# Kernel optimization log

Hardware: AMD Instinct MI355X
Metric: run time of the kernel (lower is better)

The kernel has to match this reference:

```python
import jax, jax.numpy as jnp
import numpy as np

GROUPS = 4      # DySample groups (default)
DSTATE = 16     # SSM state size
BN_EPS = 1e-5


def grid_sample_border(img, grid):
    # img: (N, C, H, W); grid: (N, Ho, Wo, 2), xy order, [-1, 1], align_corners=False,
    # padding_mode='border' (coords clamped before bilinear interp).
    N, C, H, W = img.shape
    x = jnp.clip((grid[..., 0] + 1.0) * (W * 0.5) - 0.5, 0.0, W - 1.0)
    y = jnp.clip((grid[..., 1] + 1.0) * (H * 0.5) - 0.5, 0.0, H - 1.0)
    x0 = jnp.floor(x); y0 = jnp.floor(y)
    wx = (x - x0)[:, None]; wy = (y - y0)[:, None]          # (N,1,Ho,Wo)
    x0i = x0.astype(jnp.int32); y0i = y0.astype(jnp.int32)
    x1i = jnp.minimum(x0i + 1, W - 1); y1i = jnp.minimum(y0i + 1, H - 1)
    gat = jax.vmap(lambda im, yy, xx: im[:, yy, xx])        # (C,H,W),(Ho,Wo)->(C,Ho,Wo)
    v00 = gat(img, y0i, x0i); v01 = gat(img, y0i, x1i)
    v10 = gat(img, y1i, x0i); v11 = gat(img, y1i, x1i)
    return v00 * (1 - wx) * (1 - wy) + v01 * wx * (1 - wy) + v10 * (1 - wx) * wy + v11 * wx * wy


def dysample(x, off_w, off_b, scale):
    # DySample 'lp' style (ICCV'23), groups=4, no dyscope.
    B, C, H, W = x.shape
    s, g = scale, GROUPS
    conv = jnp.einsum('bchw,co->bohw', x, off_w) + off_b[None, :, None, None]  # (B, 2*g*s*s, H, W)
    hh = ((jnp.arange(s) - (s - 1) / 2.0) / s).astype(x.dtype)                 # subpixel init positions
    ip_x = jnp.broadcast_to(hh[None, None, :], (g, s, s))
    ip_y = jnp.broadcast_to(hh[None, :, None], (g, s, s))
    ip = jnp.stack([ip_x, ip_y])                                               # (2, g, s, s)
    off = conv.reshape(B, 2, g, s, s, H, W) * 0.25 + ip[None, :, :, :, :, None, None]
    cx = jnp.arange(W, dtype=x.dtype) + 0.5
    cy = jnp.arange(H, dtype=x.dtype) + 0.5
    gx = 2.0 * (cx + off[:, 0]) / W - 1.0                                      # (B,g,s,s,H,W)
    gy = 2.0 * (cy[:, None] + off[:, 1]) / H - 1.0
    # pixel_shuffle: (B,g,si,sj,H,W) -> (B,g,H,si,W,sj) -> (B,g,sH,sW)
    gx = gx.transpose(0, 1, 4, 2, 5, 3).reshape(B, g, s * H, s * W)
    gy = gy.transpose(0, 1, 4, 2, 5, 3).reshape(B, g, s * H, s * W)
    grid = jnp.stack([gx, gy], -1).reshape(B * g, s * H, s * W, 2)
    xg = x.reshape(B * g, C // g, H, W)
    return grid_sample_border(xg, grid).reshape(B, C, s * H, s * W)


def channel_ssm(x, in_w, in_b, xproj_w, dt_w, dt_b, A_log, Dp, out_w, out_b):
    # Channel-wise bidirectional selective scan (S6) over the channel axis, gating x.
    B, C, H, W = x.shape
    n = DSTATE
    s = x.mean((-2, -1))                            # (B, C) channel descriptor
    u = s[..., None] * in_w + in_b                  # (B, C, d)
    proj = u @ xproj_w                              # (B, C, 1 + 2n)
    dt_raw = proj[..., :1]
    Bs = proj[..., 1:1 + n]
    Cs = proj[..., 1 + n:]
    dt = jax.nn.softplus(dt_raw * dt_w + dt_b)      # (B, C, d)
    A = -jnp.exp(A_log)                             # (d, n)
    dA = jnp.exp(dt[..., None] * A)                 # (B, C, d, n)
    dBu = (dt * u)[..., None] * Bs[:, :, None, :]   # (B, C, d, n)

    def scan_dir(dA_, dBu_, Cs_):
        def step(h, inp):
            a, b, c = inp
            h = a * h + b                           # (B, d, n)
            return h, jnp.einsum('bdn,bn->bd', h, c)
        h0 = jnp.zeros((B, dA_.shape[2], n), x.dtype)
        _, ys = jax.lax.scan(step, h0, (jnp.swapaxes(dA_, 0, 1), jnp.swapaxes(dBu_, 0, 1), jnp.swapaxes(Cs_, 0, 1)))
        return jnp.swapaxes(ys, 0, 1)               # (B, C, d)

    y = scan_dir(dA, dBu, Cs)
    y = y + scan_dir(dA[:, ::-1], dBu[:, ::-1], Cs[:, ::-1])[:, ::-1]
    y = y + Dp * u
    gate = jax.nn.sigmoid(y @ out_w + out_b)        # (B, C)
    return x * gate[:, :, None, None]


def setup_inputs():
    key = jax.random.key(0)
    ks = jax.random.split(key, 24)
    f = jnp.float32
    rn = lambda k, shp, sc=1.0: jax.random.normal(k, shp, dtype=f) * sc
    B = 2
    inp = {}
    inp['c1'] = rn(ks[0], (B, 96, 128, 128))
    inp['c2'] = rn(ks[1], (B, 96, 64, 64))
    inp['c3'] = rn(ks[2], (B, 192, 32, 32))
    inp['c4'] = rn(ks[3], (B, 384, 16, 16))
    inp['mlp1_w'] = rn(ks[4], (96, 384), 0.05); inp['mlp1_b'] = jnp.zeros((384,), f)
    inp['mlp2_w'] = rn(ks[5], (96, 384), 0.05); inp['mlp2_b'] = jnp.zeros((384,), f)
    inp['mlp3_w'] = rn(ks[6], (192, 384), 0.05); inp['mlp3_b'] = jnp.zeros((384,), f)
    inp['mlp4_w'] = rn(ks[7], (384, 384), 0.05); inp['mlp4_b'] = jnp.zeros((384,), f)
    inp['up2_w'] = rn(ks[8], (384, 2 * 4 * 4), 0.001); inp['up2_b'] = jnp.zeros((2 * 4 * 4,), f)
    inp['up4_w'] = rn(ks[9], (384, 2 * 4 * 16), 0.001); inp['up4_b'] = jnp.zeros((2 * 4 * 16,), f)
    inp['up8_w'] = rn(ks[10], (384, 2 * 4 * 64), 0.001); inp['up8_b'] = jnp.zeros((2 * 4 * 64,), f)
    inp['ssm_in_w'] = rn(ks[11], (64,), 0.5); inp['ssm_in_b'] = rn(ks[12], (64,), 0.1)
    inp['ssm_xproj_w'] = rn(ks[13], (64, 1 + 2 * 16), 0.1)
    inp['ssm_dt_w'] = rn(ks[14], (64,), 0.1); inp['ssm_dt_b'] = jnp.full((64,), -2.0, f)
    inp['ssm_A_log'] = jnp.log(jnp.broadcast_to(jnp.arange(1, 17, dtype=f), (64, 16)))
    inp['ssm_D'] = jnp.ones((64,), f)
    inp['ssm_out_w'] = rn(ks[15], (64,), 0.1); inp['ssm_out_b'] = jnp.zeros((), f)
    inp['fuse_w'] = rn(ks[16], (1536, 384), 0.02)
    inp['bn_g'] = jnp.ones((384,), f); inp['bn_b'] = jnp.zeros((384,), f)
    inp['bn_m'] = jnp.zeros((384,), f); inp['bn_v'] = jnp.ones((384,), f)
    inp['pred_w'] = rn(ks[17], (384, 6), 0.05); inp['pred_b'] = jnp.zeros((6,), f)
    inp['bird_w'] = rn(ks[18], (384, 2), 0.05); inp['bird_b'] = jnp.zeros((2,), f)
    return inp


def reference(c1, c2, c3, c4, mlp1_w, mlp1_b, mlp2_w, mlp2_b, mlp3_w, mlp3_b, mlp4_w, mlp4_b,
              up2_w, up2_b, up4_w, up4_b, up8_w, up8_b,
              ssm_in_w, ssm_in_b, ssm_xproj_w, ssm_dt_w, ssm_dt_b, ssm_A_log, ssm_D, ssm_out_w, ssm_out_b,
              fuse_w, bn_g, bn_b, bn_m, bn_v, pred_w, pred_b, bird_w, bird_b):
    proj = lambda c, w, b: jnp.einsum('bchw,ce->behw', c, w) + b[None, :, None, None]
    _c4 = dysample(proj(c4, mlp4_w, mlp4_b), up8_w, up8_b, 8)
    _c3 = dysample(proj(c3, mlp3_w, mlp3_b), up4_w, up4_b, 4)
    _c2 = dysample(proj(c2, mlp2_w, mlp2_b), up2_w, up2_b, 2)
    _c1 = proj(c1, mlp1_w, mlp1_b)
    cc = jnp.concatenate([_c4, _c3, _c2, _c1], axis=1)      # (B, 1536, 128, 128)
    cc = channel_ssm(cc, ssm_in_w, ssm_in_b, ssm_xproj_w, ssm_dt_w, ssm_dt_b, ssm_A_log, ssm_D, ssm_out_w, ssm_out_b)
    h = jnp.einsum('bchw,co->bohw', cc, fuse_w)             # 1x1 conv, no bias
    h = (h - bn_m[None, :, None, None]) * (bn_g / jnp.sqrt(bn_v + BN_EPS))[None, :, None, None] + bn_b[None, :, None, None]
    h = jax.nn.relu(h)                                      # dropout = identity (eval)
    out = jnp.einsum('bchw,co->bohw', h, pred_w) + pred_b[None, :, None, None]
    aux = jnp.einsum('bchw,co->bohw', h, bird_w) + bird_b[None, :, None, None]
    return (out, aux)
```

## Files before the change

### kernel.cpp

```cpp
#include <hip/hip_runtime.h>
#include <cstddef>

#define HWO 16384
#define CTOT 1536

typedef __attribute__((ext_vector_type(8))) short bf16x8;
typedef __attribute__((ext_vector_type(4))) float f32x4;

__device__ inline unsigned short f2bf(float x) {
  union { float f; unsigned u; } v; v.f = x;
  unsigned r = v.u + 0x7FFFu + ((v.u >> 16) & 1u);
  return (unsigned short)(r >> 16);
}
__device__ inline float bf2f(unsigned short h) {
  union { unsigned u; float f; } v; v.u = ((unsigned)h) << 16; return v.f;
}

struct __align__(16) Prm { unsigned short i00, i01, i10, i11; float wx, wy; };

struct SetupArgs {
  const float* W[7];
  unsigned short* T[7];
  int K[7], N[7], bstart[8];
  const float *bn_g, *bn_v, *bn_m, *bn_b;
  float *sc, *sh;
  const float* c1;
  float* mc1;
  const float* fw;
  unsigned short* fwt;
  int nTP;
};
__global__ __launch_bounds__(256) void setup_kernel(SetupArgs a) {
  int bid = blockIdx.x;
  if (bid < a.nTP) {
    int s = 0;
#pragma unroll
    for (int i = 1; i < 7; i++) if (bid >= a.bstart[i]) s = i;
    const int K = a.K[s], N = a.N[s];
    const int idx = (bid - a.bstart[s]) * 256 + threadIdx.x;
    if (idx >= K * N) return;
    const int k = idx / N, o = idx - k * N;
    a.T[s][(size_t)o * K + k] = f2bf(a.W[s][idx]);
    return;
  }
  bid -= a.nTP;
  if (bid < 2) {
    const int o = bid * 256 + threadIdx.x;
    if (o < 384) {
      const float sc = a.bn_g[o] * rsqrtf(a.bn_v[o] + 1e-5f);
      a.sc[o] = sc;
      a.sh[o] = a.bn_b[o] - a.bn_m[o] * sc;
    }
    return;
  }
  bid -= 2;
  if (bid < 192) {
    const float4* p = (const float4*)(a.c1 + (size_t)bid * HWO);
    float acc = 0.f;
    for (int i = threadIdx.x; i < HWO / 4; i += 256) {
      const float4 v = p[i];
      acc += (v.x + v.y) + (v.z + v.w);
    }
    for (int o = 32; o > 0; o >>= 1) acc += __shfl_down(acc, o, 64);
    __shared__ float red[4];
    if ((threadIdx.x & 63) == 0) red[threadIdx.x >> 6] = acc;
    __syncthreads();
    if (threadIdx.x == 0)
      a.mc1[bid] = (red[0] + red[1] + red[2] + red[3]) * (1.0f / HWO);
    return;
  }
  bid -= 192;
  const int tk = bid / 12, to = bid % 12;
  __shared__ float tile[32][33];
  const int rr0 = threadIdx.x >> 5, cch = threadIdx.x & 31;
#pragma unroll
  for (int rr = rr0; rr < 32; rr += 8)
    tile[rr][cch] = a.fw[(size_t)(tk * 32 + rr) * 384 + to * 32 + cch];
  __syncthreads();
#pragma unroll
  for (int rr = rr0; rr < 32; rr += 8)
    a.fwt[(size_t)(to * 32 + rr) * 1536 + tk * 32 + cch] = f2bf(tile[cch][rr]);
}

struct PSeg { const float* X; const unsigned short* Wt; const float* bias;
              unsigned short* Y; int P, K, blk0; };
struct PArgs { PSeg s[4]; };
__global__ __launch_bounds__(256) void proj_all(PArgs a) {
  int si = 0;
#pragma unroll
  for (int i = 1; i < 4; i++) if ((int)blockIdx.x >= a.s[i].blk0) si = i;
  const PSeg sg = a.s[si];
  const int rel = blockIdx.x - sg.blk0;
  const int pb = rel >> 1, ob = rel & 1;
  const int b = blockIdx.y;
  const int P = sg.P, K = sg.K;
  const int p0 = pb * 128;
  constexpr int LST = 40;
  __shared__ unsigned short Alds[128 * LST];
  __shared__ unsigned short Blds[192 * LST];
  const int tid = threadIdx.x;
  const int w = tid >> 6, lane = tid & 63;
  const int wm = w >> 1, wn = w & 1;
  const float* Xf = sg.X + (long)b * K * P;
  const unsigned short* Wt = sg.Wt;
  f32x4 acc[24];
#pragma unroll
  for (int i = 0; i < 24; i++) acc[i] = (f32x4){0.f, 0.f, 0.f, 0.f};
  const int lr = lane & 15, lk = (lane >> 4) * 8;

  for (int kc = 0; kc < K; kc += 32) {
#pragma unroll
    for (int it = 0; it < 4; it++) {
      const int idx = tid + it * 256;
      const int k = idx >> 5, pg = (idx & 31) * 4;
      const float4 v = *(const float4*)(Xf + (long)(kc + k) * P + p0 + pg);
      Alds[(pg + 0) * LST + k] = f2bf(v.x);
      Alds[(pg + 1) * LST + k] = f2bf(v.y);
      Alds[(pg + 2) * LST + k] = f2bf(v.z);
      Alds[(pg + 3) * LST + k] = f2bf(v.w);
    }
#pragma unroll
    for (int it = 0; it < 3; it++) {
      const int idx = tid + it * 256;
      const int r = idx >> 2, ck = (idx & 3) * 8;
      *(uint4*)&Blds[r * LST + ck] =
          *(const uint4*)(Wt + (long)(ob * 192 + r) * K + kc + ck);
    }
    __syncthreads();
    bf16x8 af[4];
#pragma unroll
    for (int mt = 0; mt < 4; mt++)
      af[mt] = *(const bf16x8*)&Alds[((wm * 4 + mt) * 16 + lr) * LST + lk];
#pragma unroll
    for (int ot = 0; ot < 6; ot++) {
      const bf16x8 bfr = *(const bf16x8*)&Blds[((wn * 6 + ot) * 16 + lr) * LST + lk];
#pragma unroll
      for (int mt = 0; mt < 4; mt++)
        acc[mt * 6 + ot] = __builtin_amdgcn_mfma_f32_16x16x32_bf16(
            af[mt], bfr, acc[mt * 6 + ot], 0, 0, 0);
    }
    __syncthreads();
  }
  const int r0 = (lane >> 4) * 4;
#pragma unroll
  for (int mt = 0; mt < 4; mt++) {
#pragma unroll
    for (int ot = 0; ot < 6; ot++) {
      const int o = ob * 192 + (wn * 6 + ot) * 16 + lr;
      const float bv = sg.bias[o];
      const f32x4 r = acc[mt * 6 + ot];
#pragma unroll
      for (int jj = 0; jj < 4; jj++) {
        const long row = p0 + (wm * 4 + mt) * 16 + r0 + jj;
        sg.Y[((long)b * P + row) * 384 + o] = f2bf(r[jj] + bv);
      }
    }
  }
}

struct OSeg { const unsigned short* X; const unsigned short* Wt;
              const float* bias; float* Y; int P, N, obn, blk0; };
struct OArgs { OSeg s[3]; };
__global__ __launch_bounds__(256) void offs_all(OArgs a) {
  int si = 0;
#pragma unroll
  for (int i = 1; i < 3; i++) if ((int)blockIdx.x >= a.s[i].blk0) si = i;
  const OSeg sg = a.s[si];
  const int rel = blockIdx.x - sg.blk0;
  const int pb = rel / sg.obn, ob = rel - pb * sg.obn;
  const int b = blockIdx.y;
  const int P = sg.P, N = sg.N;
  const int p0 = pb * 128, o0 = ob * 128;
  constexpr int LST = 40;
  __shared__ unsigned short Alds[128 * LST];
  __shared__ unsigned short Blds[128 * LST];
  const int tid = threadIdx.x;
  const int w = tid >> 6, lane = tid & 63;
  const int wm = w >> 1, wn = w & 1;
  const unsigned short* Xb = sg.X + (long)b * P * 384;
  f32x4 acc[16];
#pragma unroll
  for (int i = 0; i < 16; i++) acc[i] = (f32x4){0.f, 0.f, 0.f, 0.f};
  const int lr = lane & 15, lk = (lane >> 4) * 8;

  for (int kc = 0; kc < 384; kc += 32) {
#pragma unroll
    for (int it = 0; it < 2; it++) {
      const int idx = tid + it * 256;
      const int r = idx >> 2, ck = (idx & 3) * 8;
      *(uint4*)&Alds[r * LST + ck] =
          *(const uint4*)(Xb + (long)(p0 + r) * 384 + kc + ck);
    }
#pragma unroll
    for (int it = 0; it < 2; it++) {
      const int idx = tid + it * 256;
      const int r = idx >> 2, ck = (idx & 3) * 8;
      uint4 v = {0u, 0u, 0u, 0u};
      if (o0 + r < N)
        v = *(const uint4*)(sg.Wt + (long)(o0 + r) * 384 + kc + ck);
      *(uint4*)&Blds[r * LST + ck] = v;
    }
    __syncthreads();
    bf16x8 af[4];
#pragma unroll
    for (int mt = 0; mt < 4; mt++)
      af[mt] = *(const bf16x8*)&Alds[((wm * 4 + mt) * 16 + lr) * LST + lk];
#pragma unroll
    for (int ot = 0; ot < 4; ot++) {
      const bf16x8 bfr = *(const bf16x8*)&Blds[((wn * 4 + ot) * 16 + lr) * LST + lk];
#pragma unroll
      for (int mt = 0; mt < 4; mt++)
        acc[mt * 4 + ot] = __builtin_amdgcn_mfma_f32_16x16x32_bf16(
            af[mt], bfr, acc[mt * 4 + ot], 0, 0, 0);
    }
    __syncthreads();
  }
  const int r0 = (lane >> 4) * 4;
#pragma unroll
  for (int mt = 0; mt < 4; mt++) {
#pragma unroll
    for (int ot = 0; ot < 4; ot++) {
      const int o = o0 + (wn * 4 + ot) * 16 + lr;
      if (o < N) {
        const float bv = sg.bias[o];
        const f32x4 r = acc[mt * 4 + ot];
#pragma unroll
        for (int jj = 0; jj < 4; jj++) {
          const long row = p0 + (wm * 4 + mt) * 16 + r0 + jj;
          sg.Y[((long)b * P + row) * N + o] = r[jj] + bv;
        }
      }
    }
  }
}

__global__ __launch_bounds__(256) void pm_kernel(
    const float* __restrict__ bo4, const float* __restrict__ bo3,
    const float* __restrict__ bo2,
    const unsigned short* __restrict__ bp4, const unsigned short* __restrict__ bp3,
    const unsigned short* __restrict__ bp2,
    Prm* __restrict__ prm, float* __restrict__ part) {
  const int gp = blockIdx.y, b = blockIdx.z;
  const int lvl = gp >> 2, g = gp & 3;
  const float* bo; int ls, H, offC;
  const unsigned short* bpL; int HWs_;
  if (lvl == 0)      { bo = bo4; ls = 3; H = 16; offC = 512; bpL = bp4; HWs_ = 256; }
  else if (lvl == 1) { bo = bo3; ls = 2; H = 32; offC = 128; bpL = bp3; HWs_ = 1024; }
  else               { bo = bo2; ls = 1; H = 64; offC = 32;  bpL = bp2; HWs_ = 4096; }
  const int s = 1 << ls, ss = s * s, W = H;
  const int tid = threadIdx.x;
  __shared__ Prm Plds[512];

#pragma unroll
  for (int ii = 0; ii < 2; ii++) {
    const int li = tid + ii * 256;
    const int p = blockIdx.x * 512 + li;
    const int yo = p >> 7, xo = p & 127;
    const int h = yo >> ls, i = yo & (s - 1);
    const int w = xo >> ls, j = xo & (s - 1);
    const int sp = h * W + w;
    const float* offp = bo + ((size_t)b * (W * H) + sp) * offC;
    const float cx = offp[g * ss + i * s + j];
    const float cy = offp[(4 + g) * ss + i * s + j];
    const float inv_s = 1.0f / (float)s;
    const float offx = cx * 0.25f + ((float)j - (s - 1) * 0.5f) * inv_s;
    const float offy = cy * 0.25f + ((float)i - (s - 1) * 0.5f) * inv_s;
    float xf = fminf(fmaxf((float)w + offx, 0.0f), (float)(W - 1));
    float yf = fminf(fmaxf((float)h + offy, 0.0f), (float)(H - 1));
    const float x0f = floorf(xf), y0f = floorf(yf);
    const int x0 = (int)x0f, y0 = (int)y0f;
    const int x1 = min(x0 + 1, W - 1), y1 = min(y0 + 1, H - 1);
    Prm pr;
    pr.i00 = (unsigned short)(y0 * W + x0);
    pr.i01 = (unsigned short)(y0 * W + x1);
    pr.i10 = (unsigned short)(y1 * W + x0);
    pr.i11 = (unsigned short)(y1 * W + x1);
    pr.wx = xf - x0f;
    pr.wy = yf - y0f;
    prm[((size_t)b * 12 + gp) * HWO + p] = pr;
    Plds[li] = pr;
  }
  __syncthreads();

  const int chunk = tid % 12, pl = tid / 12;
  float acc[8];
#pragma unroll
  for (int j = 0; j < 8; j++) acc[j] = 0.f;
  const unsigned short* qb = bpL + (size_t)b * HWs_ * 384 + g * 96 + chunk * 8;
  if (tid < 252) {
    for (int it = 0; it < 25; it++) {
      const int pli = it * 21 + pl;
      if (pli < 512) {
        const Prm pr = Plds[pli];
        const float wx = pr.wx, wy = pr.wy;
        const float w00 = (1.f - wx) * (1.f - wy), w01 = wx * (1.f - wy);
        const float w10 = (1.f - wx) * wy, w11 = wx * wy;
        const uint4 v00 = *(const uint4*)(qb + (size_t)pr.i00 * 384);
        const uint4 v01 = *(const uint4*)(qb + (size_t)pr.i01 * 384);
        const uint4 v10 = *(const uint4*)(qb + (size_t)pr.i10 * 384);
        const uint4 v11 = *(const uint4*)(qb + (size_t)pr.i11 * 384);
        const unsigned short* s00 = (const unsigned short*)&v00;
        const unsigned short* s01 = (const unsigned short*)&v01;
        const unsigned short* s10 = (const unsigned short*)&v10;
        const unsigned short* s11 = (const unsigned short*)&v11;
#pragma unroll
        for (int j = 0; j < 8; j++)
          acc[j] += w00 * bf2f(s00[j]) + w01 * bf2f(s01[j]) +
                    w10 * bf2f(s10[j]) + w11 * bf2f(s11[j]);
      }
    }
  }
  __shared__ float red[12][8][22];
  if (tid < 252) {
#pragma unroll
    for (int j = 0; j < 8; j++) red[chunk][j][pl] = acc[j];
  }
  __syncthreads();
  if (tid < 96) {
    float sum = 0.f;
#pragma unroll
    for (int l = 0; l < 21; l++) sum += red[tid >> 3][tid & 7][l];
    part[((size_t)blockIdx.x * 2 + b) * 1152 + gp * 96 + tid] = sum;
  }
}

__global__ __launch_bounds__(64) void ssm_prep(
    const float* __restrict__ part, const float* __restrict__ mc1,
    const float* __restrict__ mlp1_w, const float* __restrict__ mlp1_b,
    const float* __restrict__ in_w, const float* __restrict__ in_b,
    const float* __restrict__ xproj_w, const float* __restrict__ dt_w,
    const float* __restrict__ dt_b, float* __restrict__ u_out,
    float2* __restrict__ dtdu_out, float* __restrict__ Bs_out,
    float* __restrict__ Cs_out) {
  const int bc = blockIdx.x;
  const int b = bc / 1536, c = bc - b * 1536;
  const int d = threadIdx.x;
  float sv;
  if (c < 1152) {
    float a = (d < 32) ? part[((size_t)d * 2 + b) * 1152 + c] : 0.f;
    a += __shfl_xor(a, 1, 64);  a += __shfl_xor(a, 2, 64);
    a += __shfl_xor(a, 4, 64);  a += __shfl_xor(a, 8, 64);
    a += __shfl_xor(a, 16, 64); a += __shfl_xor(a, 32, 64);
    sv = a * (1.0f / HWO);
  } else {
    const int c2 = c - 1152;
    float a = mc1[b * 96 + d] * mlp1_w[d * 384 + c2];
    if (d < 32) a += mc1[b * 96 + 64 + d] * mlp1_w[(64 + d) * 384 + c2];
    a += __shfl_xor(a, 1, 64);  a += __shfl_xor(a, 2, 64);
    a += __shfl_xor(a, 4, 64);  a += __shfl_xor(a, 8, 64);
    a += __shfl_xor(a, 16, 64); a += __shfl_xor(a, 32, 64);
    sv = a + mlp1_b[c2];
  }
  const float u = sv * in_w[d] + in_b[d];
  __shared__ float ush[64];
  __shared__ float proj[33];
  ush[d] = u;
  __syncthreads();
  if (d < 33) {
    float acc = 0.f;
    for (int k = 0; k < 64; k++) acc = fmaf(ush[k], xproj_w[k * 33 + d], acc);
    proj[d] = acc;
  }
  __syncthreads();
  float dtv = proj[0] * dt_w[d] + dt_b[d];
  dtv = (dtv > 20.0f) ? dtv : log1pf(__expf(dtv));
  u_out[(size_t)bc * 64 + d] = u;
  dtdu_out[(size_t)bc * 64 + d] = make_float2(dtv, dtv * u);
  if (d < 16) {
    Bs_out[(size_t)bc * 16 + d] = proj[1 + d];
    Cs_out[(size_t)bc * 16 + d] = proj[17 + d];
  }
}

__global__ __launch_bounds__(256) void ssm_scan_par(
    const float2* __restrict__ dtdu, const float* __restrict__ Bs,
    const float* __restrict__ Cs, const float* __restrict__ A_log,
    float* __restrict__ y) {
  const int d = blockIdx.x, dir = blockIdx.y, b = blockIdx.z;
  const int t = threadIdx.x;
  const int j = t >> 4, n = t & 15;
  const float A = -__expf(A_log[d * 16 + n]);
  const int s0 = j * 96;
  const int c0 = dir ? (1535 - s0) : s0;
  const int step = dir ? -1 : 1;
  const float2* dbase = dtdu + (size_t)b * 1536 * 64 + (size_t)c0 * 64 + d;
  const float* bbase = Bs + (size_t)b * 1536 * 16 + (size_t)c0 * 16 + n;
  const float* cbase = Cs + (size_t)b * 1536 * 16 + (size_t)c0 * 16 + n;
  const long dstep = (long)step * 64;
  const long bstep = (long)step * 16;

  float Ap = 1.f, Bp = 0.f;
  {
    const float2* dp = dbase;
    const float* bp = bbase;
    float2 td = *dp;
    float Bv = *bp;
    for (int i = 0; i < 96; i++) {
      const float2 tdc = td;
      const float Bc = Bv;
      dp += dstep; bp += bstep;
      if (i + 1 < 96) { td = *dp; Bv = *bp; }
      const float a = __expf(tdc.x * A);
      Bp = fmaf(a, Bp, tdc.y * Bc);
      Ap *= a;
    }
  }
  __shared__ float sA[16][16], sB[16][16];
  sA[j][n] = Ap;
  sB[j][n] = Bp;
  __syncthreads();
  float H = 0.f;
  for (int jj = 0; jj < j; jj++) H = fmaf(sA[jj][n], H, sB[jj][n]);

  float* yb = y + (size_t)(b * 2 + dir) * 1536 * 64;
  {
    const float2* dp = dbase;
    const float* bp = bbase;
    const float* cp = cbase;
    float2 td = *dp;
    float Bv = *bp;
    float Cv = *cp;
    float h = H;
    int c = c0;
    for (int i = 0; i < 96; i++) {
      const float2 tdc = td;
      const float Bc = Bv, Cc = Cv;
      dp += dstep; bp += bstep; cp += bstep;
      if (i + 1 < 96) { td = *dp; Bv = *bp; Cv = *cp; }
      const float a = __expf(tdc.x * A);
      h = fmaf(a, h, tdc.y * Bc);
      float pr = h * Cc;
      pr += __shfl_xor(pr, 1, 64);
      pr += __shfl_xor(pr, 2, 64);
      pr += __shfl_xor(pr, 4, 64);
      pr += __shfl_xor(pr, 8, 64);
      if (n == 0) yb[(size_t)c * 64 + d] = pr;
      c += step;
    }
  }
}

__global__ __launch_bounds__(64) void gate_kernel(
    const float* __restrict__ y, const float* __restrict__ u,
    const float* __restrict__ Dp, const float* __restrict__ out_w,
    const float* __restrict__ out_b, float* __restrict__ gate) {
  const int c = blockIdx.x, b = blockIdx.y, d = threadIdx.x;
  const size_t i = ((size_t)b * 1536 + c) * 64 + d;
  float yt = y[((size_t)(b * 2) * 1536 + c) * 64 + d]
           + y[((size_t)(b * 2 + 1) * 1536 + c) * 64 + d]
           + Dp[d] * u[i];
  float v = yt * out_w[d];
  for (int o = 32; o > 0; o >>= 1) v += __shfl_down(v, o, 64);
  if (d == 0) gate[b * 1536 + c] = 1.0f / (1.0f + __expf(-(v + out_b[0])));
}

__global__ __launch_bounds__(256) void gate_fold(
    const unsigned short* __restrict__ wtf, const float* __restrict__ gate,
    unsigned short* __restrict__ wg) {
  const int b = blockIdx.y;
  const int idx8 = blockIdx.x * 256 + threadIdx.x;
  const int o = idx8 / 192;
  const int k0 = (idx8 - o * 192) * 8;
  const size_t idx = (size_t)o * 1536 + k0;
  const uint4 v = *(const uint4*)(wtf + idx);
  const unsigned short* s = (const unsigned short*)&v;
  const float* g = gate + b * 1536 + k0;
  unsigned short r8[8];
#pragma unroll
  for (int j = 0; j < 8; j++) r8[j] = f2bf(bf2f(s[j]) * g[j]);
  *(uint4*)(wg + (size_t)b * 589824 + idx) = *(const uint4*)r8;
}

__global__ __launch_bounds__(1024, 4) void fuse_gemm(
    const unsigned short* __restrict__ bp4, const unsigned short* __restrict__ bp3,
    const unsigned short* __restrict__ bp2, const unsigned short* __restrict__ bp1,
    const Prm* __restrict__ prm, const unsigned short* __restrict__ wg,
    const float* __restrict__ ep_a, const float* __restrict__ ep_b,
    unsigned short* __restrict__ hbf) {
  constexpr int LST = 36;
  __shared__ unsigned short Alds[128 * LST];
  __shared__ unsigned short Blds[384 * LST];
  const int tid = threadIdx.x;
  const int w = tid >> 6, lane = tid & 63;
  const int wm = w >> 2, wn = w & 3;
  const int b = blockIdx.y;
  const int p0 = blockIdx.x * 128;
  const unsigned short* Wb = wg + (size_t)b * 589824;
  f32x4 acc[12];
#pragma unroll
  for (int i = 0; i < 12; i++) acc[i] = (f32x4){0.f, 0.f, 0.f, 0.f};
  const int lr = lane & 15, lk = (lane >> 4) * 8;
  const int ar = tid >> 2, ag = tid & 3;

  for (int gp = 0; gp < 12; ++gp) {
    const int lvl = gp >> 2;
    const unsigned short* bpL; int HWs_;
    if (lvl == 0)      { bpL = bp4; HWs_ = 256; }
    else if (lvl == 1) { bpL = bp3; HWs_ = 1024; }
    else               { bpL = bp2; HWs_ = 4096; }
    Prm pr; pr.i00 = pr.i01 = pr.i10 = pr.i11 = 0; pr.wx = pr.wy = 0.f;
    if (tid < 512) pr = prm[((size_t)b * 12 + gp) * HWO + p0 + ar];
    const float wx = pr.wx, wy = pr.wy;
    const float w00 = (1.f - wx) * (1.f - wy), w01 = wx * (1.f - wy);
    const float w10 = (1.f - wx) * wy, w11 = wx * wy;
#pragma unroll
    for (int t3 = 0; t3 < 3; ++t3) {
      const int kc = gp * 96 + t3 * 32;
      if (tid < 512) {
        const int colL = (gp & 3) * 96 + t3 * 32 + ag * 8;
        const unsigned short* qb = bpL + (size_t)b * HWs_ * 384 + colL;
        const uint4 v00 = *(const uint4*)(qb + (size_t)pr.i00 * 384);
        const uint4 v01 = *(const uint4*)(qb + (size_t)pr.i01 * 384);
        const uint4 v10 = *(const uint4*)(qb + (size_t)pr.i10 * 384);
        const uint4 v11 = *(const uint4*)(qb + (size_t)pr.i11 * 384);
        const unsigned short* s00 = (const unsigned short*)&v00;
        const unsigned short* s01 = (const unsigned short*)&v01;
        const unsigned short* s10 = (const unsigned short*)&v10;
        const unsigned short* s11 = (const unsigned short*)&v11;
        unsigned short r8[8];
#pragma unroll
        for (int jj = 0; jj < 8; jj++)
          r8[jj] = f2bf(w00 * bf2f(s00[jj]) + w01 * bf2f(s01[jj]) +
                        w10 * bf2f(s10[jj]) + w11 * bf2f(s11[jj]));
        *(uint4*)&Alds[ar * LST + ag * 8] = *(const uint4*)r8;
      }
      {
        const int r = tid >> 2, ck = (tid & 3) * 8;
        *(uint4*)&Blds[r * LST + ck] =
            *(const uint4*)(Wb + (size_t)r * 1536 + kc + ck);
      }
      if (tid >= 512) {
        const int idx = tid + 512;
        const int r = idx >> 2, ck = (idx & 3) * 8;
        *(uint4*)&Blds[r * LST + ck] =
            *(const uint4*)(Wb + (size_t)r * 1536 + kc + ck);
      }
      __syncthreads();
      bf16x8 af[2];
#pragma unroll
      for (int mt = 0; mt < 2; mt++)
        af[mt] = *(const bf16x8*)&Alds[((wm * 2 + mt) * 16 + lr) * LST + lk];
#pragma unroll
      for (int ot = 0; ot < 6; ot++) {
        const bf16x8 bfr = *(const bf16x8*)&Blds[((wn * 6 + ot) * 16 + lr) * LST + lk];
#pragma unroll
        for (int mt = 0; mt < 2; mt++)
          acc[mt * 6 + ot] = __builtin_amdgcn_mfma_f32_16x16x32_bf16(
              af[mt], bfr, acc[mt * 6 + ot], 0, 0, 0);
      }
      __syncthreads();
    }
  }
  for (int kc = 1152; kc < 1536; kc += 32) {
    if (tid < 512)
      *(uint4*)&Alds[ar * LST + ag * 8] =
          *(const uint4*)(bp1 + ((size_t)b * HWO + p0 + ar) * 384 +
                          (kc - 1152) + ag * 8);
    {
      const int r = tid >> 2, ck = (tid & 3) * 8;
      *(uint4*)&Blds[r * LST + ck] =
          *(const uint4*)(Wb + (size_t)r * 1536 + kc + ck);
    }
    if (tid >= 512) {
      const int idx = tid + 512;
      const int r = idx >> 2, ck = (idx & 3) * 8;
      *(uint4*)&Blds[r * LST + ck] =
          *(const uint4*)(Wb + (size_t)r * 1536 + kc + ck);
    }
    __syncthreads();
    bf16x8 af[2];
#pragma unroll
    for (int mt = 0; mt < 2; mt++)
      af[mt] = *(const bf16x8*)&Alds[((wm * 2 + mt) * 16 + lr) * LST + lk];
#pragma unroll
    for (int ot = 0; ot < 6; ot++) {
      const bf16x8 bfr = *(const bf16x8*)&Blds[((wn * 6 + ot) * 16 + lr) * LST + lk];
#pragma unroll
      for (int mt = 0; mt < 2; mt++)
        acc[mt * 6 + ot] = __builtin_amdgcn_mfma_f32_16x16x32_bf16(
            af[mt], bfr, acc[mt * 6 + ot], 0, 0, 0);
    }
    __syncthreads();
  }
  const int r0 = (lane >> 4) * 4;
#pragma unroll
  for (int mt = 0; mt < 2; mt++) {
#pragma unroll
    for (int ot = 0; ot < 6; ot++) {
      const int o = (wn * 6 + ot) * 16 + lr;
      const float sa = ep_a[o], sb = ep_b[o];
      const f32x4 r = acc[mt * 6 + ot];
#pragma unroll
      for (int jj = 0; jj < 4; jj++) {
        const size_t row = p0 + (wm * 2 + mt) * 16 + r0 + jj;
        hbf[((size_t)b * HWO + row) * 384 + o] =
            f2bf(fmaxf(fmaf(r[jj], sa, sb), 0.f));
      }
    }
  }
}

__global__ __launch_bounds__(256) void head_pm(
    const unsigned short* __restrict__ h,
    const float* __restrict__ pred_w, const float* __restrict__ pred_b,
    const float* __restrict__ bird_w, const float* __restrict__ bird_b,
    float* __restrict__ out) {
  const int idx = blockIdx.x * 256 + threadIdx.x;
  const int b = idx >> 14, p = idx & 16383;
  const unsigned short* hb = h + ((size_t)b * HWO + p) * 384;
  float a0 = pred_b[0], a1 = pred_b[1], a2 = pred_b[2];
  float a3 = pred_b[3], a4 = pred_b[4], a5 = pred_b[5];
  float a6 = bird_b[0], a7 = bird_b[1];
  for (int c8 = 0; c8 < 384; c8 += 8) {
    const uint4 v = *(const uint4*)(hb + c8);
    const unsigned short* sv = (const unsigned short*)&v;
#pragma unroll
    for (int jj = 0; jj < 8; jj++) {
      const int o = c8 + jj;
      const float hv = bf2f(sv[jj]);
      const float* pw = pred_w + o * 6;
      a0 = fmaf(hv, pw[0], a0);
      a1 = fmaf(hv, pw[1], a1);
      a2 = fmaf(hv, pw[2], a2);
      a3 = fmaf(hv, pw[3], a3);
      a4 = fmaf(hv, pw[4], a4);
      a5 = fmaf(hv, pw[5], a5);
      a6 = fmaf(hv, bird_w[o * 2 + 0], a6);
      a7 = fmaf(hv, bird_w[o * 2 + 1], a7);
    }
  }
  float* ob = out + (size_t)b * 6 * HWO + p;
  ob[0] = a0; ob[HWO] = a1; ob[2 * HWO] = a2;
  ob[3 * HWO] = a3; ob[4 * HWO] = a4; ob[5 * HWO] = a5;
  float* ab = out + (size_t)12 * HWO + (size_t)b * 2 * HWO + p;
  ab[0] = a6; ab[HWO] = a7;
}

extern "C" void kernel_launch(void* const* d_in, const int* in_sizes, int n_in,
                              void* d_out, int out_size, void* d_ws, size_t ws_size,
                              hipStream_t stream) {
  const float* c1      = (const float*)d_in[0];
  const float* c2      = (const float*)d_in[1];
  const float* c3      = (const float*)d_in[2];
  const float* c4      = (const float*)d_in[3];
  const float* mlp1_w  = (const float*)d_in[4];
  const float* mlp1_b  = (const float*)d_in[5];
  const float* mlp2_w  = (const float*)d_in[6];
  const float* mlp2_b  = (const float*)d_in[7];
  const float* mlp3_w  = (const float*)d_in[8];
  const float* mlp3_b  = (const float*)d_in[9];
  const float* mlp4_w  = (const float*)d_in[10];
  const float* mlp4_b  = (const float*)d_in[11];
  const float* up2_w   = (const float*)d_in[12];
  const float* up2_b   = (const float*)d_in[13];
  const float* up4_w   = (const float*)d_in[14];
  const float* up4_b   = (const float*)d_in[15];
  const float* up8_w   = (const float*)d_in[16];
  const float* up8_b   = (const float*)d_in[17];
  const float* ssm_in_w    = (const float*)d_in[18];
  const float* ssm_in_b    = (const float*)d_in[19];
  const float* ssm_xproj_w = (const float*)d_in[20];
  const float* ssm_dt_w    = (const float*)d_in[21];
  const float* ssm_dt_b    = (const float*)d_in[22];
  const float* ssm_A_log   = (const float*)d_in[23];
  const float* ssm_D       = (const float*)d_in[24];
  const float* ssm_out_w   = (const float*)d_in[25];
  const float* ssm_out_b   = (const float*)d_in[26];
  const float* fuse_w  = (const float*)d_in[27];
  const float* bn_g    = (const float*)d_in[28];
  const float* bn_b    = (const float*)d_in[29];
  const float* bn_m    = (const float*)d_in[30];
  const float* bn_v    = (const float*)d_in[31];
  const float* pred_w  = (const float*)d_in[32];
  const float* pred_b  = (const float*)d_in[33];
  const float* bird_w  = (const float*)d_in[34];
  const float* bird_b  = (const float*)d_in[35];
  float* outp = (float*)d_out;
  (void)in_sizes; (void)n_in; (void)out_size; (void)ws_size;

  float* ws = (float*)d_ws;
  size_t off = 0;
  auto alloc = [&](size_t n) { float* p = ws + off; off += n; return p; };
  unsigned short* bp1 = (unsigned short*)alloc(6291456);
  unsigned short* bp4 = (unsigned short*)alloc(98304);
  unsigned short* bp3 = (unsigned short*)alloc(393216);
  unsigned short* bp2 = (unsigned short*)alloc(1572864);
  float* bo4 = alloc(262144);
  float* bo3 = alloc(262144);
  float* bo2 = alloc(262144);
  Prm* prm = (Prm*)alloc(1572864);
  float* part = alloc(73728);
  float* mc1  = alloc(192);
  float* ub   = alloc(196608);
  float2* dtdu = (float2*)alloc(393216);
  float* Bsb  = alloc(49152);
  float* Csb  = alloc(49152);
  float* yb   = alloc(393216);
  float* gteb = alloc(3072);
  float* scb  = alloc(384);
  float* shb  = alloc(384);
  unsigned short* hbf = (unsigned short*)alloc(6291456);
  unsigned short* t1  = (unsigned short*)(ws + off);
  unsigned short* t2  = t1 + 36864;
  unsigned short* t3  = t2 + 36864;
  unsigned short* t4  = t3 + 73728;
  unsigned short* t8  = t4 + 147456;
  unsigned short* t4u = t8 + 196608;
  unsigned short* t2u = t4u + 49152;
  unsigned short* wtf = t2u + 12288;
  unsigned short* wg  = wtf + 589824;

  {
    SetupArgs sp;
    const float* Ws[7] = {mlp1_w, mlp2_w, mlp3_w, mlp4_w, up8_w, up4_w, up2_w};
    unsigned short* Ts[7] = {t1, t2, t3, t4, t8, t4u, t2u};
    const int Ks[7] = {96, 96, 192, 384, 384, 384, 384};
    const int Ns[7] = {384, 384, 384, 384, 512, 128, 32};
    int bs = 0;
    for (int i = 0; i < 7; i++) {
      sp.W[i] = Ws[i]; sp.T[i] = Ts[i]; sp.K[i] = Ks[i]; sp.N[i] = Ns[i];
      sp.bstart[i] = bs;
      bs += (Ks[i] * Ns[i] + 255) / 256;
    }
    sp.bstart[7] = bs;
    sp.nTP = bs;
    sp.bn_g = bn_g; sp.bn_v = bn_v; sp.bn_m = bn_m; sp.bn_b = bn_b;
    sp.sc = scb; sp.sh = shb;
    sp.c1 = c1; sp.mc1 = mc1;
    sp.fw = fuse_w; sp.fwt = wtf;
    hipLaunchKernelGGL(setup_kernel, dim3(bs + 2 + 192 + 576), dim3(256), 0, stream, sp);
  }

  {
    PArgs pa;
    pa.s[0] = {c4, t4, mlp4_b, bp4, 256, 384, 0};
    pa.s[1] = {c3, t3, mlp3_b, bp3, 1024, 192, 4};
    pa.s[2] = {c2, t2, mlp2_b, bp2, 4096, 96, 20};
    pa.s[3] = {c1, t1, mlp1_b, bp1, 16384, 96, 84};
    hipLaunchKernelGGL(proj_all, dim3(340, 2), dim3(256), 0, stream, pa);
  }
  {
    OArgs oa;
    oa.s[0] = {bp4, t8, up8_b, bo4, 256, 512, 4, 0};
    oa.s[1] = {bp3, t4u, up4_b, bo3, 1024, 128, 1, 8};
    oa.s[2] = {bp2, t2u, up2_b, bo2, 4096, 32, 1, 16};
    hipLaunchKernelGGL(offs_all, dim3(48, 2), dim3(256), 0, stream, oa);
  }
  hipLaunchKernelGGL(pm_kernel, dim3(32, 12, 2), dim3(256), 0, stream,
                     bo4, bo3, bo2, bp4, bp3, bp2, prm, part);
  hipLaunchKernelGGL(ssm_prep, dim3(3072), dim3(64), 0, stream,
                     part, mc1, mlp1_w, mlp1_b, ssm_in_w, ssm_in_b,
                     ssm_xproj_w, ssm_dt_w, ssm_dt_b, ub, dtdu, Bsb, Csb);
  hipLaunchKernelGGL(ssm_scan_par, dim3(64, 2, 2), dim3(256), 0, stream,
                     dtdu, Bsb, Csb, ssm_A_log, yb);
  hipLaunchKernelGGL(gate_kernel, dim3(1536, 2), dim3(64), 0, stream,
                     yb, ub, ssm_D, ssm_out_w, ssm_out_b, gteb);
  hipLaunchKernelGGL(gate_fold, dim3(288, 2), dim3(256), 0, stream, wtf, gteb, wg);
  hipLaunchKernelGGL(fuse_gemm, dim3(128, 2), dim3(1024), 0, stream,
                     bp4, bp3, bp2, bp1, prm, wg, scb, shb, hbf);
  hipLaunchKernelGGL(head_pm, dim3(128), dim3(256), 0, stream,
                     hbf, pred_w, pred_b, bird_w, bird_b, outp);
}
```

Baseline: 224.4 us.

## Apply SSM gate to activation panels and share weights across batch in fuse GEMM

The per-batch channel gate is no longer folded into a per-batch copy of the fuse weights. It is instead applied in place to the projected activation panels (bp1..bp4) before the GEMM. This lets a single fuse_gemm block handle both batch elements with one shared weight tile loaded into LDS, doubling the A tile and the accumulators to 24. Weight traffic is halved, all 1024 threads now gather, and the grid shrinks from 256 to 128 blocks. The cost is higher register pressure (min-occupancy hint removed), fewer blocks to fill the GPU, and an extra read-modify-write pass over all activation panels, which are larger than the weights.

```diff
diff --git a/kernel.cpp b/kernel.cpp
--- a/kernel.cpp
+++ b/kernel.cpp
@@ -454,43 +454,48 @@
   if (d == 0) gate[b * 1536 + c] = 1.0f / (1.0f + __expf(-(v + out_b[0])));
 }
 
-__global__ __launch_bounds__(256) void gate_fold(
-    const unsigned short* __restrict__ wtf, const float* __restrict__ gate,
-    unsigned short* __restrict__ wg) {
-  const int b = blockIdx.y;
-  const int idx8 = blockIdx.x * 256 + threadIdx.x;
-  const int o = idx8 / 192;
-  const int k0 = (idx8 - o * 192) * 8;
-  const size_t idx = (size_t)o * 1536 + k0;
-  const uint4 v = *(const uint4*)(wtf + idx);
+__global__ __launch_bounds__(256) void gate_panels(
+    unsigned short* __restrict__ bp1, unsigned short* __restrict__ bp2,
+    unsigned short* __restrict__ bp3, unsigned short* __restrict__ bp4,
+    const float* __restrict__ gate) {
+  const int bid = blockIdx.x;
+  unsigned short* ptr; int base, P, rel;
+  if (bid < 6144)      { ptr = bp1; base = 1152; P = 16384; rel = bid; }
+  else if (bid < 7680) { ptr = bp2; base = 768;  P = 4096;  rel = bid - 6144; }
+  else if (bid < 8064) { ptr = bp3; base = 384;  P = 1024;  rel = bid - 7680; }
+  else                 { ptr = bp4; base = 0;    P = 256;   rel = bid - 8064; }
+  const int i = rel * 256 + threadIdx.x;
+  const int row = i / 48, cg = (i - row * 48) * 8;
+  const int b = (row >= P) ? 1 : 0;
+  const float* g = gate + b * 1536 + base + cg;
+  uint4 v = *(uint4*)(ptr + (size_t)i * 8);
   const unsigned short* s = (const unsigned short*)&v;
-  const float* g = gate + b * 1536 + k0;
   unsigned short r8[8];
 #pragma unroll
   for (int j = 0; j < 8; j++) r8[j] = f2bf(bf2f(s[j]) * g[j]);
-  *(uint4*)(wg + (size_t)b * 589824 + idx) = *(const uint4*)r8;
-}
-
-__global__ __launch_bounds__(1024, 4) void fuse_gemm(
+  *(uint4*)(ptr + (size_t)i * 8) = *(const uint4*)r8;
+}
+
+__global__ __launch_bounds__(1024) void fuse_gemm(
     const unsigned short* __restrict__ bp4, const unsigned short* __restrict__ bp3,
     const unsigned short* __restrict__ bp2, const unsigned short* __restrict__ bp1,
-    const Prm* __restrict__ prm, const unsigned short* __restrict__ wg,
+    const Prm* __restrict__ prm, const unsigned short* __restrict__ wtf,
     const float* __restrict__ ep_a, const float* __restrict__ ep_b,
     unsigned short* __restrict__ hbf) {
   constexpr int LST = 36;
-  __shared__ unsigned short Alds[128 * LST];
+  __shared__ unsigned short Alds[256 * LST];
   __shared__ unsigned short Blds[384 * LST];
   const int tid = threadIdx.x;
   const int w = tid >> 6, lane = tid & 63;
   const int wm = w >> 2, wn = w & 3;
-  const int b = blockIdx.y;
   const int p0 = blockIdx.x * 128;
-  const unsigned short* Wb = wg + (size_t)b * 589824;
-  f32x4 acc[12];
-#pragma unroll
-  for (int i = 0; i < 12; i++) acc[i] = (f32x4){0.f, 0.f, 0.f, 0.f};
+  f32x4 acc[24];
+#pragma unroll
+  for (int i = 0; i < 24; i++) acc[i] = (f32x4){0.f, 0.f, 0.f, 0.f};
   const int lr = lane & 15, lk = (lane >> 4) * 8;
-  const int ar = tid >> 2, ag = tid & 3;
+  const int half = tid >> 9;
+  const int st = tid & 511;
+  const int ar = st >> 2, ag = st & 3;
 
   for (int gp = 0; gp < 12; ++gp) {
     const int lvl = gp >> 2;
@@ -498,17 +503,16 @@
     if (lvl == 0)      { bpL = bp4; HWs_ = 256; }
     else if (lvl == 1) { bpL = bp3; HWs_ = 1024; }
     else               { bpL = bp2; HWs_ = 4096; }
-    Prm pr; pr.i00 = pr.i01 = pr.i10 = pr.i11 = 0; pr.wx = pr.wy = 0.f;
-    if (tid < 512) pr = prm[((size_t)b * 12 + gp) * HWO + p0 + ar];
+    const Prm pr = prm[((size_t)half * 12 + gp) * HWO + p0 + ar];
     const float wx = pr.wx, wy = pr.wy;
     const float w00 = (1.f - wx) * (1.f - wy), w01 = wx * (1.f - wy);
     const float w10 = (1.f - wx) * wy, w11 = wx * wy;
 #pragma unroll
     for (int t3 = 0; t3 < 3; ++t3) {
       const int kc = gp * 96 + t3 * 32;
-      if (tid < 512) {
+      {
         const int colL = (gp & 3) * 96 + t3 * 32 + ag * 8;
-        const unsigned short* qb = bpL + (size_t)b * HWs_ * 384 + colL;
+        const unsigned short* qb = bpL + (size_t)half * HWs_ * 384 + colL;
         const uint4 v00 = *(const uint4*)(qb + (size_t)pr.i00 * 384);
         const uint4 v01 = *(const uint4*)(qb + (size_t)pr.i01 * 384);
         const uint4 v10 = *(const uint4*)(qb + (size_t)pr.i10 * 384);
@@ -522,79 +526,87 @@
         for (int jj = 0; jj < 8; jj++)
           r8[jj] = f2bf(w00 * bf2f(s00[jj]) + w01 * bf2f(s01[jj]) +
                         w10 * bf2f(s10[jj]) + w11 * bf2f(s11[jj]));
-        *(uint4*)&Alds[ar * LST + ag * 8] = *(const uint4*)r8;
+        *(uint4*)&Alds[(half * 128 + ar) * LST + ag * 8] = *(const uint4*)r8;
       }
       {
         const int r = tid >> 2, ck = (tid & 3) * 8;
         *(uint4*)&Blds[r * LST + ck] =
-            *(const uint4*)(Wb + (size_t)r * 1536 + kc + ck);
+            *(const uint4*)(wtf + (size_t)r * 1536 + kc + ck);
       }
       if (tid >= 512) {
         const int idx = tid + 512;
         const int r = idx >> 2, ck = (idx & 3) * 8;
         *(uint4*)&Blds[r * LST + ck] =
-            *(const uint4*)(Wb + (size_t)r * 1536 + kc + ck);
+            *(const uint4*)(wtf + (size_t)r * 1536 + kc + ck);
       }
       __syncthreads();
-      bf16x8 af[2];
-#pragma unroll
-      for (int mt = 0; mt < 2; mt++)
-        af[mt] = *(const bf16x8*)&Alds[((wm * 2 + mt) * 16 + lr) * LST + lk];
-#pragma unroll
-      for (int ot = 0; ot < 6; ot++) {
-        const bf16x8 bfr = *(const bf16x8*)&Blds[((wn * 6 + ot) * 16 + lr) * LST + lk];
+#pragma unroll
+      for (int bt = 0; bt < 2; bt++) {
+        bf16x8 af[2];
 #pragma unroll
         for (int mt = 0; mt < 2; mt++)
-          acc[mt * 6 + ot] = __builtin_amdgcn_mfma_f32_16x16x32_bf16(
-              af[mt], bfr, acc[mt * 6 + ot], 0, 0, 0);
+          af[mt] = *(const bf16x8*)&Alds[(bt * 128 + (wm * 2 + mt) * 16 + lr) * LST + lk];
+#pragma unroll
+        for (int ot = 0; ot < 6; ot++) {
+          const bf16x8 bfr = *(const bf16x8*)&Blds[((wn * 6 + ot) * 16 + lr) * LST + lk];
+#pragma unroll
+          for (int mt = 0; mt < 2; mt++)
+            acc[bt * 12 + mt * 6 + ot] = __builtin_amdgcn_mfma_f32_16x16x32_bf16(
+                af[mt], bfr, acc[bt * 12 + mt * 6 + ot], 0, 0, 0);
+        }
       }
       __syncthreads();
     }
   }
   for (int kc = 1152; kc < 1536; kc += 32) {
-    if (tid < 512)
-      *(uint4*)&Alds[ar * LST + ag * 8] =
-          *(const uint4*)(bp1 + ((size_t)b * HWO + p0 + ar) * 384 +
-                          (kc - 1152) + ag * 8);
+    *(uint4*)&Alds[(half * 128 + ar) * LST + ag * 8] =
+        *(const uint4*)(bp1 + ((size_t)half * HWO + p0 + ar) * 384 +
+                        (kc - 1152) + ag * 8);
     {
       const int r = tid >> 2, ck = (tid & 3) * 8;
       *(uint4*)&Blds[r * LST + ck] =
-          *(const uint4*)(Wb + (size_t)r * 1536 + kc + ck);
+          *(const uint4*)(wtf + (size_t)r * 1536 + kc + ck);
     }
     if (tid >= 512) {
       const int idx = tid + 512;
       const int r = idx >> 2, ck = (idx & 3) * 8;
       *(uint4*)&Blds[r * LST + ck] =
-          *(const uint4*)(Wb + (size_t)r * 1536 + kc + ck);
+          *(const uint4*)(wtf + (size_t)r * 1536 + kc + ck);
     }
     __syncthreads();
-    bf16x8 af[2];
-#pragma unroll
-    for (int mt = 0; mt < 2; mt++)
-      af[mt] = *(const bf16x8*)&Alds[((wm * 2 + mt) * 16 + lr) * LST + lk];
-#pragma unroll
-    for (int ot = 0; ot < 6; ot++) {
-      const bf16x8 bfr = *(const bf16x8*)&Blds[((wn * 6 + ot) * 16 + lr) * LST + lk];
+#pragma unroll
+    for (int bt = 0; bt < 2; bt++) {
+      bf16x8 af[2];
 #pragma unroll
       for (int mt = 0; mt < 2; mt++)
-        acc[mt * 6 + ot] = __builtin_amdgcn_mfma_f32_16x16x32_bf16(
-            af[mt], bfr, acc[mt * 6 + ot], 0, 0, 0);
+        af[mt] = *(const bf16x8*)&Alds[(bt * 128 + (wm * 2 + mt) * 16 + lr) * LST + lk];
+#pragma unroll
+      for (int ot = 0; ot < 6; ot++) {
+        const bf16x8 bfr = *(const bf16x8*)&Blds[((wn * 6 + ot) * 16 + lr) * LST + lk];
+#pragma unroll
+        for (int mt = 0; mt < 2; mt++)
+          acc[bt * 12 + mt * 6 + ot] = __builtin_amdgcn_mfma_f32_16x16x32_bf16(
+              af[mt], bfr, acc[bt * 12 + mt * 6 + ot], 0, 0, 0);
+      }
     }
     __syncthreads();
   }
   const int r0 = (lane >> 4) * 4;
 #pragma unroll
-  for (int mt = 0; mt < 2; mt++) {
-#pragma unroll
-    for (int ot = 0; ot < 6; ot++) {
-      const int o = (wn * 6 + ot) * 16 + lr;
-      const float sa = ep_a[o], sb = ep_b[o];
-      const f32x4 r = acc[mt * 6 + ot];
-#pragma unroll
-      for (int jj = 0; jj < 4; jj++) {
-        const size_t row = p0 + (wm * 2 + mt) * 16 + r0 + jj;
-        hbf[((size_t)b * HWO + row) * 384 + o] =
-            f2bf(fmaxf(fmaf(r[jj], sa, sb), 0.f));
+  for (int bt = 0; bt < 2; bt++) {
+#pragma unroll
+    for (int mt = 0; mt < 2; mt++) {
+#pragma unroll
+      for (int ot = 0; ot < 6; ot++) {
+        const int o = (wn * 6 + ot) * 16 + lr;
+        const float sa = ep_a[o], sb = ep_b[o];
+        const f32x4 r = acc[bt * 12 + mt * 6 + ot];
+#pragma unroll
+        for (int jj = 0; jj < 4; jj++) {
+          const size_t row = p0 + (wm * 2 + mt) * 16 + r0 + jj;
+          hbf[((size_t)bt * HWO + row) * 384 + o] =
+              f2bf(fmaxf(fmaf(r[jj], sa, sb), 0.f));
+        }
       }
     }
   }
@@ -708,7 +720,6 @@
   unsigned short* t4u = t8 + 196608;
   unsigned short* t2u = t4u + 49152;
   unsigned short* wtf = t2u + 12288;
-  unsigned short* wg  = wtf + 589824;
 
   {
     SetupArgs sp;
@@ -755,9 +766,10 @@
                      dtdu, Bsb, Csb, ssm_A_log, yb);
   hipLaunchKernelGGL(gate_kernel, dim3(1536, 2), dim3(64), 0, stream,
                      yb, ub, ssm_D, ssm_out_w, ssm_out_b, gteb);
-  hipLaunchKernelGGL(gate_fold, dim3(288, 2), dim3(256), 0, stream, wtf, gteb, wg);
-  hipLaunchKernelGGL(fuse_gemm, dim3(128, 2), dim3(1024), 0, stream,
-                     bp4, bp3, bp2, bp1, prm, wg, scb, shb, hbf);
+  hipLaunchKernelGGL(gate_panels, dim3(8160), dim3(256), 0, stream,
+                     bp1, bp2, bp3, bp4, gteb);
+  hipLaunchKernelGGL(fuse_gemm, dim3(128), dim3(1024), 0, stream,
+                     bp4, bp3, bp2, bp1, prm, wtf, scb, shb, hbf);
   hipLaunchKernelGGL(head_pm, dim3(128), dim3(256), 0, stream,
                      hbf, pred_w, pred_b, bird_w, bird_b, outp);
 }
```

New measurement: 674.1 us. 3x slower.
